# Kernel optimization log

Hardware: AMD Instinct MI355X
Metric: run time of the kernel (lower is better)

## Reference

```python
import jax, jax.numpy as jnp
import numpy as np

B, S, D, E, F = 2, 1024, 1024, 14, 2048

def setup_inputs() -> dict:
    key = jax.random.key(0)
    k0, k1, k2, k3 = jax.random.split(key, 4)
    h = jax.random.normal(k0, (B, S, D), jnp.float32)
    gate_w = jax.random.normal(k1, (E, D), jnp.float32) * 0.02
    # kaiming-uniform-ish scale for expert weights
    w1 = jax.random.normal(k2, (E, D, F), jnp.float32) * (1.0 / np.sqrt(D).astype(np.float32))
    b1 = jnp.zeros((E, F), jnp.float32)
    w2 = jax.random.normal(k3, (E, F, D), jnp.float32) * (1.0 / np.sqrt(F).astype(np.float32))
    b2 = jnp.zeros((E, D), jnp.float32)
    return {"h": h, "gate_w": gate_w, "w1": w1, "b1": b1, "w2": w2, "b2": b2}

def reference(h, gate_w, w1, b1, w2, b2):
    # Eval-mode forward (no expert dropout, router_step=None, return_aux=False path)
    Bb, Ss, Dd = h.shape
    x = h.reshape(Bb * Ss, Dd)                       # (N, D)
    logits = x @ gate_w.T                            # (N, E)
    probs = jax.nn.softmax(logits, axis=-1)
    top2_p, top2_i = jax.lax.top_k(probs, 2)         # (N, 2)
    w = top2_p / jnp.maximum(top2_p.sum(-1, keepdims=True), 1e-10)
    # dense all-experts FFN
    hh = jnp.einsum('nd,edf->nef', x, w1) + b1       # (N, E, F)
    hh = jax.nn.gelu(hh, approximate=False)          # torch F.gelu default = exact erf
    all_out = jnp.einsum('nef,efd->ned', hh, w2) + b2  # (N, E, D)
    n = jnp.arange(x.shape[0])
    out0 = all_out[n, top2_i[:, 0]]                  # (N, D)
    out1 = all_out[n, top2_i[:, 1]]
    moe_out = w[:, 0:1] * out0 + w[:, 1:2] * out1
    result = jnp.clip(x + moe_out, -100.0, 100.0).reshape(Bb, Ss, Dd)
    return result
```

## Files before the change

### kernel.cpp

```cpp
#include <hip/hip_runtime.h>
#include <cstdint>
#include <cstddef>

#define NTOK 2048
#define DDIM 1024
#define FDIM 2048
#define NEXP 14
#define MAXT 2048

typedef __attribute__((ext_vector_type(8))) short short8;
typedef __attribute__((ext_vector_type(4))) float floatx4;

__device__ __forceinline__ unsigned pack2bf(float lo, float hi) {
    unsigned a = __float_as_uint(lo), b = __float_as_uint(hi);
    return ((a + 0x8000u) >> 16) | ((b + 0x8000u) & 0xffff0000u);
}
__device__ __forceinline__ unsigned short f2bf1(float f) {
    return (unsigned short)((__float_as_uint(f) + 0x8000u) >> 16);
}

__device__ __forceinline__ void glds16(const void* g, void* lds) {
    __builtin_amdgcn_global_load_lds((const __attribute__((address_space(1))) unsigned*)g,
                                     (__attribute__((address_space(3))) unsigned*)lds, 16, 0, 0);
}

__device__ __forceinline__ int bswz(int n) { return ((n >> 2) ^ n ^ (n >> 4)) & 7; }

__global__ __launch_bounds__(256) void cvtx_kernel(const float* __restrict__ x,
                                                   unsigned short* __restrict__ xb,
                                                   int* __restrict__ cnt) {
    if (blockIdx.x == 0 && threadIdx.x < NEXP) cnt[threadIdx.x] = 0;
    const size_t i = ((size_t)blockIdx.x * 256 + threadIdx.x) * 8;
    float4 a = *(const float4*)(x + i);
    float4 b = *(const float4*)(x + i + 4);
    uint4 u;
    u.x = pack2bf(a.x, a.y); u.y = pack2bf(a.z, a.w);
    u.z = pack2bf(b.x, b.y); u.w = pack2bf(b.z, b.w);
    *(uint4*)(xb + i) = u;
}

__global__ __launch_bounds__(256) void gate_kernel(
    const float* __restrict__ x, const float* __restrict__ gw,
    int* __restrict__ cnt, int* __restrict__ lists, float* __restrict__ wt)
{
    const int wave = threadIdx.x >> 6, lane = threadIdx.x & 63;
    const int n = blockIdx.x * 4 + wave;
    float part[NEXP];
#pragma unroll
    for (int e = 0; e < NEXP; ++e) part[e] = 0.f;
    const float4* xr = (const float4*)(x + (size_t)n * DDIM);
#pragma unroll
    for (int kk = 0; kk < 4; ++kk) {
        const float4 xv = xr[kk * 64 + lane];
#pragma unroll
        for (int e = 0; e < NEXP; ++e) {
            const float4 g = ((const float4*)(gw + e * DDIM))[kk * 64 + lane];
            part[e] = fmaf(xv.x, g.x, fmaf(xv.y, g.y, fmaf(xv.z, g.z, fmaf(xv.w, g.w, part[e]))));
        }
    }
#pragma unroll
    for (int e = 0; e < NEXP; ++e) {
        float v = part[e];
        for (int off = 32; off; off >>= 1) v += __shfl_xor(v, off);
        part[e] = v;
    }
    int i0 = 0; float l0 = part[0];
#pragma unroll
    for (int e = 1; e < NEXP; ++e) if (part[e] > l0) { l0 = part[e]; i0 = e; }
    int i1 = -1; float l1 = -3.0e38f;
#pragma unroll
    for (int e = 0; e < NEXP; ++e) if (e != i0 && part[e] > l1) { l1 = part[e]; i1 = e; }
    if (lane == 0) {
        const float r  = __expf(l1 - l0);
        wt[2 * n]     = 1.f / (1.f + r);
        wt[2 * n + 1] = r / (1.f + r);
        int p0 = atomicAdd(&cnt[i0], 1); lists[i0 * MAXT + p0] = 2 * n;
        int p1 = atomicAdd(&cnt[i1], 1); lists[i1 * MAXT + p1] = 2 * n + 1;
    }
}

#define MAXJOBS 78
__global__ void jobs_kernel(const int* __restrict__ cnt, int* __restrict__ job_e,
                            int* __restrict__ job_mt, int* __restrict__ njobs) {
    if (threadIdx.x == 0) {
        int J = 0;
        for (int e = 0; e < NEXP; ++e) {
            const int m = (cnt[e] + 63) >> 6;
            for (int i = 0; i < m; ++i) { job_e[J] = e; job_mt[J] = i; ++J; }
        }
        njobs[0] = J;
    }
}

__global__ __launch_bounds__(256) void gemm1_kernel(
    const unsigned short* __restrict__ xb, const float* __restrict__ w1,
    const float* __restrict__ b1, const int* __restrict__ cnt,
    const int* __restrict__ lists, const int* __restrict__ job_e,
    const int* __restrict__ job_mt, const int* __restrict__ njobs,
    unsigned short* __restrict__ hh)
{
    const int j = blockIdx.y;
    if (j >= njobs[0]) return;
    const int e = job_e[j], mt = job_mt[j], nt = blockIdx.x;
    const int count = cnt[e];
    const int* list = lists + e * MAXT + mt * 64;
    const int mloc = min(64, count - mt * 64);

    __shared__ __align__(16) unsigned short As[2][64 * 64];
    __shared__ __align__(16) unsigned short Bs[2][128 * 64];

    const int t = threadIdx.x, lane = t & 63, wave = t >> 6;
    const int lrow = lane & 15, lq = lane >> 4;
    const int wm = (wave & 1) * 32, wn = (wave >> 1) * 64;

    const int achk = (lane & 7) ^ (lane >> 3);
    const int r0 = wave * 16 + (lane >> 3);
    const unsigned short* aG0 = xb + (size_t)(list[min(r0, mloc - 1)] >> 1) * DDIM + achk * 8;
    const unsigned short* aG1 = xb + (size_t)(list[min(r0 + 8, mloc - 1)] >> 1) * DDIM + achk * 8;

    const int n4 = (t & 31) * 4, kg = t >> 5;
    const float* bG = w1 + (size_t)e * DDIM * FDIM + nt * 128 + n4;

    floatx4 acc[2][4];
#pragma unroll
    for (int i = 0; i < 2; ++i)
#pragma unroll
        for (int jn = 0; jn < 4; ++jn) acc[i][jn] = (floatx4)0.f;

    floatx4 brv[8];
    glds16(aG0, &As[0][(wave * 16) * 64]);
    glds16(aG1, &As[0][(wave * 16 + 8) * 64]);
#pragma unroll
    for (int jj = 0; jj < 8; ++jj)
        brv[jj] = *(const floatx4*)(bG + (size_t)(kg * 8 + jj) * FDIM);
#pragma unroll
    for (int nn = 0; nn < 4; ++nn) {
        const int n = n4 + nn, slot = kg ^ bswz(n);
        uint4 u;
        u.x = pack2bf(brv[0][nn], brv[1][nn]); u.y = pack2bf(brv[2][nn], brv[3][nn]);
        u.z = pack2bf(brv[4][nn], brv[5][nn]); u.w = pack2bf(brv[6][nn], brv[7][nn]);
        *(uint4*)&Bs[0][n * 64 + slot * 8] = u;
    }
#pragma unroll
    for (int jj = 0; jj < 8; ++jj)
        brv[jj] = *(const floatx4*)(bG + (size_t)(64 + kg * 8 + jj) * FDIM);

    int p = 0;
    for (int k0 = 0; k0 < DDIM; k0 += 64) {
        __syncthreads();
        if (k0 + 64 < DDIM) {
            glds16(aG0 + k0 + 64, &As[p ^ 1][(wave * 16) * 64]);
            glds16(aG1 + k0 + 64, &As[p ^ 1][(wave * 16 + 8) * 64]);
#pragma unroll
            for (int nn = 0; nn < 4; ++nn) {
                const int n = n4 + nn, slot = kg ^ bswz(n);
                uint4 u;
                u.x = pack2bf(brv[0][nn], brv[1][nn]); u.y = pack2bf(brv[2][nn], brv[3][nn]);
                u.z = pack2bf(brv[4][nn], brv[5][nn]); u.w = pack2bf(brv[6][nn], brv[7][nn]);
                *(uint4*)&Bs[p ^ 1][n * 64 + slot * 8] = u;
            }
        }
        if (k0 + 128 < DDIM) {
#pragma unroll
            for (int jj = 0; jj < 8; ++jj)
                brv[jj] = *(const floatx4*)(bG + (size_t)(k0 + 128 + kg * 8 + jj) * FDIM);
        }
#pragma unroll
        for (int ks = 0; ks < 2; ++ks) {
            const int c = ks * 4 + lq;
            short8 af[2], bf[4];
#pragma unroll
            for (int i = 0; i < 2; ++i) {
                const int r = wm + i * 16 + lrow;
                af[i] = *(const short8*)&As[p][r * 64 + ((c ^ (r & 7)) * 8)];
            }
#pragma unroll
            for (int jn = 0; jn < 4; ++jn) {
                const int n = wn + jn * 16 + lrow;
                bf[jn] = *(const short8*)&Bs[p][n * 64 + ((c ^ bswz(n)) * 8)];
            }
#pragma unroll
            for (int i = 0; i < 2; ++i)
#pragma unroll
                for (int jn = 0; jn < 4; ++jn)
                    acc[i][jn] = __builtin_amdgcn_mfma_f32_16x16x32_bf16(af[i], bf[jn], acc[i][jn], 0, 0, 0);
        }
        p ^= 1;
    }
#pragma unroll
    for (int jn = 0; jn < 4; ++jn) {
        const int n = nt * 128 + wn + jn * 16 + lrow;
        const float bias = b1[e * FDIM + n];
#pragma unroll
        for (int i = 0; i < 2; ++i) {
#pragma unroll
            for (int r = 0; r < 4; ++r) {
                const int m = wm + i * 16 + lq * 4 + r;
                if (m < mloc) {
                    const int pp = list[m];
                    float v = acc[i][jn][r] + bias;
                    v = 0.5f * v * (1.0f + erff(v * 0.70710678118654752f));
                    hh[(size_t)pp * FDIM + n] = f2bf1(v);
                }
            }
        }
    }
}

__global__ __launch_bounds__(256) void gemm2_kernel(
    const unsigned short* __restrict__ hh, const float* __restrict__ w2,
    const float* __restrict__ b2, const int* __restrict__ cnt,
    const int* __restrict__ lists, const int* __restrict__ job_e,
    const int* __restrict__ job_mt, const int* __restrict__ njobs,
    const float* __restrict__ wt, float* __restrict__ out0, float* __restrict__ out1)
{
    const int j = blockIdx.y;
    if (j >= njobs[0]) return;
    const int e = job_e[j], mt = job_mt[j], nt = blockIdx.x;
    const int count = cnt[e];
    const int* list = lists + e * MAXT + mt * 64;
    const int mloc = min(64, count - mt * 64);

    __shared__ __align__(16) unsigned short As[2][64 * 64];
    __shared__ __align__(16) unsigned short Bs[2][128 * 64];

    const int t = threadIdx.x, lane = t & 63, wave = t >> 6;
    const int lrow = lane & 15, lq = lane >> 4;
    const int wm = (wave & 1) * 32, wn = (wave >> 1) * 64;

    const int achk = (lane & 7) ^ (lane >> 3);
    const int r0 = wave * 16 + (lane >> 3);
    const unsigned short* aG0 = hh + (size_t)list[min(r0, mloc - 1)] * FDIM + achk * 8;
    const unsigned short* aG1 = hh + (size_t)list[min(r0 + 8, mloc - 1)] * FDIM + achk * 8;

    const int n4 = (t & 31) * 4, kg = t >> 5;
    const float* bG = w2 + (size_t)e * FDIM * DDIM + nt * 128 + n4;

    floatx4 acc[2][4];
#pragma unroll
    for (int i = 0; i < 2; ++i)
#pragma unroll
        for (int jn = 0; jn < 4; ++jn) acc[i][jn] = (floatx4)0.f;

    floatx4 brv[8];
    glds16(aG0, &As[0][(wave * 16) * 64]);
    glds16(aG1, &As[0][(wave * 16 + 8) * 64]);
#pragma unroll
    for (int jj = 0; jj < 8; ++jj)
        brv[jj] = *(const floatx4*)(bG + (size_t)(kg * 8 + jj) * DDIM);
#pragma unroll
    for (int nn = 0; nn < 4; ++nn) {
        const int n = n4 + nn, slot = kg ^ bswz(n);
        uint4 u;
        u.x = pack2bf(brv[0][nn], brv[1][nn]); u.y = pack2bf(brv[2][nn], brv[3][nn]);
        u.z = pack2bf(brv[4][nn], brv[5][nn]); u.w = pack2bf(brv[6][nn], brv[7][nn]);
        *(uint4*)&Bs[0][n * 64 + slot * 8] = u;
    }
#pragma unroll
    for (int jj = 0; jj < 8; ++jj)
        brv[jj] = *(const floatx4*)(bG + (size_t)(64 + kg * 8 + jj) * DDIM);

    int p = 0;
    for (int k0 = 0; k0 < FDIM; k0 += 64) {
        __syncthreads();
        if (k0 + 64 < FDIM) {
            glds16(aG0 + k0 + 64, &As[p ^ 1][(wave * 16) * 64]);
            glds16(aG1 + k0 + 64, &As[p ^ 1][(wave * 16 + 8) * 64]);
#pragma unroll
            for (int nn = 0; nn < 4; ++nn) {
                const int n = n4 + nn, slot = kg ^ bswz(n);
                uint4 u;
                u.x = pack2bf(brv[0][nn], brv[1][nn]); u.y = pack2bf(brv[2][nn], brv[3][nn]);
                u.z = pack2bf(brv[4][nn], brv[5][nn]); u.w = pack2bf(brv[6][nn], brv[7][nn]);
                *(uint4*)&Bs[p ^ 1][n * 64 + slot * 8] = u;
            }
        }
        if (k0 + 128 < FDIM) {
#pragma unroll
            for (int jj = 0; jj < 8; ++jj)
                brv[jj] = *(const floatx4*)(bG + (size_t)(k0 + 128 + kg * 8 + jj) * DDIM);
        }
#pragma unroll
        for (int ks = 0; ks < 2; ++ks) {
            const int c = ks * 4 + lq;
            short8 af[2], bf[4];
#pragma unroll
            for (int i = 0; i < 2; ++i) {
                const int r = wm + i * 16 + lrow;
                af[i] = *(const short8*)&As[p][r * 64 + ((c ^ (r & 7)) * 8)];
            }
#pragma unroll
            for (int jn = 0; jn < 4; ++jn) {
                const int n = wn + jn * 16 + lrow;
                bf[jn] = *(const short8*)&Bs[p][n * 64 + ((c ^ bswz(n)) * 8)];
            }
#pragma unroll
            for (int i = 0; i < 2; ++i)
#pragma unroll
                for (int jn = 0; jn < 4; ++jn)
                    acc[i][jn] = __builtin_amdgcn_mfma_f32_16x16x32_bf16(af[i], bf[jn], acc[i][jn], 0, 0, 0);
        }
        p ^= 1;
    }
#pragma unroll
    for (int jn = 0; jn < 4; ++jn) {
        const int n = nt * 128 + wn + jn * 16 + lrow;
        const float bias = b2[e * DDIM + n];
#pragma unroll
        for (int i = 0; i < 2; ++i) {
#pragma unroll
            for (int r = 0; r < 4; ++r) {
                const int m = wm + i * 16 + lq * 4 + r;
                if (m < mloc) {
                    const int pp = list[m];
                    const int tok = pp >> 1;
                    const float v = (acc[i][jn][r] + bias) * wt[pp];
                    float* dst = (pp & 1) ? out1 : out0;
                    dst[(size_t)tok * DDIM + n] = v;
                }
            }
        }
    }
}

__global__ __launch_bounds__(256) void finalize_kernel(
    const float* __restrict__ x, const float* __restrict__ o1,
    float* __restrict__ out)
{
    const size_t i = ((size_t)blockIdx.x * 256 + threadIdx.x) * 4;
    float4 xv = *(const float4*)(x + i);
    float4 a  = *(const float4*)(out + i);
    float4 b  = *(const float4*)(o1 + i);
    float4 r;
    r.x = fminf(fmaxf(xv.x + a.x + b.x, -100.f), 100.f);
    r.y = fminf(fmaxf(xv.y + a.y + b.y, -100.f), 100.f);
    r.z = fminf(fmaxf(xv.z + a.z + b.z, -100.f), 100.f);
    r.w = fminf(fmaxf(xv.w + a.w + b.w, -100.f), 100.f);
    *(float4*)(out + i) = r;
}

extern "C" void kernel_launch(void* const* d_in, const int* in_sizes, int n_in,
                              void* d_out, int out_size, void* d_ws, size_t ws_size,
                              hipStream_t stream) {
    const float* h  = (const float*)d_in[0];
    const float* gw = (const float*)d_in[1];
    const float* w1 = (const float*)d_in[2];
    const float* b1 = (const float*)d_in[3];
    const float* w2 = (const float*)d_in[4];
    const float* b2 = (const float*)d_in[5];
    float* out = (float*)d_out;

    char* ws = (char*)d_ws;
    int*   cnt    = (int*)ws;
    int*   lists  = (int*)(ws + 256);
    float* wt     = (float*)(ws + 114944);
    int*   job_e  = (int*)(ws + 131328);
    int*   job_mt = (int*)(ws + 131840);
    int*   njobs  = (int*)(ws + 132352);
    unsigned short* xb = (unsigned short*)(ws + 262144);
    float* o1     = (float*)(ws + 262144 + 4194304);
    unsigned short* hhb = (unsigned short*)(ws + 262144 + 4194304 + 8388608);

    cvtx_kernel<<<NTOK * DDIM / (256 * 8), 256, 0, stream>>>(h, xb, cnt);
    gate_kernel<<<NTOK / 4, 256, 0, stream>>>(h, gw, cnt, lists, wt);
    jobs_kernel<<<1, 64, 0, stream>>>(cnt, job_e, job_mt, njobs);
    gemm1_kernel<<<dim3(FDIM / 128, MAXJOBS), 256, 0, stream>>>(xb, w1, b1, cnt, lists, job_e, job_mt, njobs, hhb);
    gemm2_kernel<<<dim3(DDIM / 128, MAXJOBS), 256, 0, stream>>>(hhb, w2, b2, cnt, lists, job_e, job_mt, njobs, wt, out, o1);
    finalize_kernel<<<NTOK * DDIM / (256 * 4), 256, 0, stream>>>(h, o1, out);
}
```

Before: 414.7 us.

## Software-pipeline expert GEMM main loops with partial waitcnt and MFMA priority

Both expert GEMM K-loops are rewritten as a manually unrolled two-stage pipeline with ping-pong register buffers for the fp32 weight prefetch. Each step waits with `s_waitcnt vmcnt(8)` before a raw `s_barrier`, rather than a full `__syncthreads`. This lets the next tile's weight global loads stay in flight across the barrier, hiding memory latency behind MFMA work. Sched barriers fix the instruction order, `s_setprio` raises wave priority around the MFMA bursts, and launch bounds request 3 blocks per CU. The risks are higher register pressure from the doubled prefetch buffers and correctness relying on hand-counted vmcnt values.

```diff
diff --git a/kernel.cpp b/kernel.cpp
--- a/kernel.cpp
+++ b/kernel.cpp
@@ -25,6 +25,8 @@
 }
 
 __device__ __forceinline__ int bswz(int n) { return ((n >> 2) ^ n ^ (n >> 4)) & 7; }
+
+#define SBAR() __builtin_amdgcn_sched_barrier(0)
 
 __global__ __launch_bounds__(256) void cvtx_kernel(const float* __restrict__ x,
                                                    unsigned short* __restrict__ xb,
@@ -92,7 +94,49 @@
     }
 }
 
-__global__ __launch_bounds__(256) void gemm1_kernel(
+#define LOADB(dst, kbase, STRIDE) {                                           \
+    _Pragma("unroll") for (int jj = 0; jj < 8; ++jj)                          \
+        dst[jj] = *(const floatx4*)(bG + (size_t)((kbase) + kg * 8 + jj) * (STRIDE)); }
+
+#define WRITEB(src, buf) {                                                    \
+    _Pragma("unroll") for (int nn = 0; nn < 4; ++nn) {                        \
+        const int n_ = n4 + nn, slot_ = kg ^ bswz(n_);                        \
+        uint4 u_;                                                             \
+        u_.x = pack2bf(src[0][nn], src[1][nn]); u_.y = pack2bf(src[2][nn], src[3][nn]); \
+        u_.z = pack2bf(src[4][nn], src[5][nn]); u_.w = pack2bf(src[6][nn], src[7][nn]); \
+        *(uint4*)&Bs[buf][n_ * 64 + slot_ * 8] = u_; } }
+
+#define STAGEA(buf, koff) {                                                   \
+    glds16(aG0 + (koff), &As[buf][(wave * 16) * 64]);                         \
+    glds16(aG1 + (koff), &As[buf][(wave * 16 + 8) * 64]); }
+
+#define COMPUTE(buf) {                                                        \
+    _Pragma("unroll") for (int ks = 0; ks < 2; ++ks) {                        \
+        const int c_ = ks * 4 + lq;                                           \
+        short8 af[2], bf[4];                                                  \
+        _Pragma("unroll") for (int ii = 0; ii < 2; ++ii) {                    \
+            const int r_ = wm + ii * 16 + lrow;                               \
+            af[ii] = *(const short8*)&As[buf][r_ * 64 + ((c_ ^ (r_ & 7)) * 8)]; } \
+        _Pragma("unroll") for (int jn = 0; jn < 4; ++jn) {                    \
+            const int n_ = wn + jn * 16 + lrow;                               \
+            bf[jn] = *(const short8*)&Bs[buf][n_ * 64 + ((c_ ^ bswz(n_)) * 8)]; } \
+        __builtin_amdgcn_s_setprio(1);                                        \
+        _Pragma("unroll") for (int ii = 0; ii < 2; ++ii)                      \
+            _Pragma("unroll") for (int jn = 0; jn < 4; ++jn)                  \
+                acc[ii][jn] = __builtin_amdgcn_mfma_f32_16x16x32_bf16(af[ii], bf[jn], acc[ii][jn], 0, 0, 0); \
+        __builtin_amdgcn_s_setprio(0); } }
+
+#define STEADY(i, curbuf, brv_c, brv_n, STRIDE) {                             \
+    STAGEA((curbuf) ^ 1, ((i) + 1) * 64);                                     \
+    WRITEB(brv_c, (curbuf) ^ 1);                                              \
+    SBAR();                                                                   \
+    LOADB(brv_n, ((i) + 2) * 64, STRIDE);                                     \
+    SBAR();                                                                   \
+    COMPUTE(curbuf);                                                          \
+    asm volatile("s_waitcnt vmcnt(8) lgkmcnt(0)" ::: "memory");               \
+    __builtin_amdgcn_s_barrier(); }
+
+__global__ __launch_bounds__(256, 3) void gemm1_kernel(
     const unsigned short* __restrict__ xb, const float* __restrict__ w1,
     const float* __restrict__ b1, const int* __restrict__ cnt,
     const int* __restrict__ lists, const int* __restrict__ job_e,
@@ -123,82 +167,47 @@
 
     floatx4 acc[2][4];
 #pragma unroll
-    for (int i = 0; i < 2; ++i)
-#pragma unroll
-        for (int jn = 0; jn < 4; ++jn) acc[i][jn] = (floatx4)0.f;
-
-    floatx4 brv[8];
-    glds16(aG0, &As[0][(wave * 16) * 64]);
-    glds16(aG1, &As[0][(wave * 16 + 8) * 64]);
-#pragma unroll
-    for (int jj = 0; jj < 8; ++jj)
-        brv[jj] = *(const floatx4*)(bG + (size_t)(kg * 8 + jj) * FDIM);
-#pragma unroll
-    for (int nn = 0; nn < 4; ++nn) {
-        const int n = n4 + nn, slot = kg ^ bswz(n);
-        uint4 u;
-        u.x = pack2bf(brv[0][nn], brv[1][nn]); u.y = pack2bf(brv[2][nn], brv[3][nn]);
-        u.z = pack2bf(brv[4][nn], brv[5][nn]); u.w = pack2bf(brv[6][nn], brv[7][nn]);
-        *(uint4*)&Bs[0][n * 64 + slot * 8] = u;
-    }
-#pragma unroll
-    for (int jj = 0; jj < 8; ++jj)
-        brv[jj] = *(const floatx4*)(bG + (size_t)(64 + kg * 8 + jj) * FDIM);
-
-    int p = 0;
-    for (int k0 = 0; k0 < DDIM; k0 += 64) {
-        __syncthreads();
-        if (k0 + 64 < DDIM) {
-            glds16(aG0 + k0 + 64, &As[p ^ 1][(wave * 16) * 64]);
-            glds16(aG1 + k0 + 64, &As[p ^ 1][(wave * 16 + 8) * 64]);
-#pragma unroll
-            for (int nn = 0; nn < 4; ++nn) {
-                const int n = n4 + nn, slot = kg ^ bswz(n);
-                uint4 u;
-                u.x = pack2bf(brv[0][nn], brv[1][nn]); u.y = pack2bf(brv[2][nn], brv[3][nn]);
-                u.z = pack2bf(brv[4][nn], brv[5][nn]); u.w = pack2bf(brv[6][nn], brv[7][nn]);
-                *(uint4*)&Bs[p ^ 1][n * 64 + slot * 8] = u;
-            }
-        }
-        if (k0 + 128 < DDIM) {
-#pragma unroll
-            for (int jj = 0; jj < 8; ++jj)
-                brv[jj] = *(const floatx4*)(bG + (size_t)(k0 + 128 + kg * 8 + jj) * FDIM);
-        }
-#pragma unroll
-        for (int ks = 0; ks < 2; ++ks) {
-            const int c = ks * 4 + lq;
-            short8 af[2], bf[4];
-#pragma unroll
-            for (int i = 0; i < 2; ++i) {
-                const int r = wm + i * 16 + lrow;
-                af[i] = *(const short8*)&As[p][r * 64 + ((c ^ (r & 7)) * 8)];
-            }
-#pragma unroll
-            for (int jn = 0; jn < 4; ++jn) {
-                const int n = wn + jn * 16 + lrow;
-                bf[jn] = *(const short8*)&Bs[p][n * 64 + ((c ^ bswz(n)) * 8)];
-            }
-#pragma unroll
-            for (int i = 0; i < 2; ++i)
-#pragma unroll
-                for (int jn = 0; jn < 4; ++jn)
-                    acc[i][jn] = __builtin_amdgcn_mfma_f32_16x16x32_bf16(af[i], bf[jn], acc[i][jn], 0, 0, 0);
-        }
-        p ^= 1;
-    }
+    for (int ii = 0; ii < 2; ++ii)
+#pragma unroll
+        for (int jn = 0; jn < 4; ++jn) acc[ii][jn] = (floatx4)0.f;
+
+    floatx4 brvA[8], brvB[8];
+
+    STAGEA(0, 0);
+    SBAR();
+    LOADB(brvB, 0, FDIM);
+    WRITEB(brvB, 0);
+    SBAR();
+    LOADB(brvA, 64, FDIM);
+    asm volatile("s_waitcnt vmcnt(8) lgkmcnt(0)" ::: "memory");
+    __builtin_amdgcn_s_barrier();
+
+#pragma unroll 1
+    for (int it = 0; it < 7; ++it) {
+        const int i = it * 2;
+        STEADY(i, 0, brvA, brvB, FDIM);
+        STEADY(i + 1, 1, brvB, brvA, FDIM);
+    }
+    STAGEA(1, 15 * 64);
+    WRITEB(brvA, 1);
+    SBAR();
+    COMPUTE(0);
+    asm volatile("s_waitcnt vmcnt(0) lgkmcnt(0)" ::: "memory");
+    __builtin_amdgcn_s_barrier();
+    COMPUTE(1);
+
 #pragma unroll
     for (int jn = 0; jn < 4; ++jn) {
         const int n = nt * 128 + wn + jn * 16 + lrow;
         const float bias = b1[e * FDIM + n];
 #pragma unroll
-        for (int i = 0; i < 2; ++i) {
+        for (int ii = 0; ii < 2; ++ii) {
 #pragma unroll
             for (int r = 0; r < 4; ++r) {
-                const int m = wm + i * 16 + lq * 4 + r;
+                const int m = wm + ii * 16 + lq * 4 + r;
                 if (m < mloc) {
                     const int pp = list[m];
-                    float v = acc[i][jn][r] + bias;
+                    float v = acc[ii][jn][r] + bias;
                     v = 0.5f * v * (1.0f + erff(v * 0.70710678118654752f));
                     hh[(size_t)pp * FDIM + n] = f2bf1(v);
                 }
@@ -207,7 +216,7 @@
     }
 }
 
-__global__ __launch_bounds__(256) void gemm2_kernel(
+__global__ __launch_bounds__(256, 3) void gemm2_kernel(
     const unsigned short* __restrict__ hh, const float* __restrict__ w2,
     const float* __restrict__ b2, const int* __restrict__ cnt,
     const int* __restrict__ lists, const int* __restrict__ job_e,
@@ -238,83 +247,48 @@
 
     floatx4 acc[2][4];
 #pragma unroll
-    for (int i = 0; i < 2; ++i)
-#pragma unroll
-        for (int jn = 0; jn < 4; ++jn) acc[i][jn] = (floatx4)0.f;
-
-    floatx4 brv[8];
-    glds16(aG0, &As[0][(wave * 16) * 64]);
-    glds16(aG1, &As[0][(wave * 16 + 8) * 64]);
-#pragma unroll
-    for (int jj = 0; jj < 8; ++jj)
-        brv[jj] = *(const floatx4*)(bG + (size_t)(kg * 8 + jj) * DDIM);
-#pragma unroll
-    for (int nn = 0; nn < 4; ++nn) {
-        const int n = n4 + nn, slot = kg ^ bswz(n);
-        uint4 u;
-        u.x = pack2bf(brv[0][nn], brv[1][nn]); u.y = pack2bf(brv[2][nn], brv[3][nn]);
-        u.z = pack2bf(brv[4][nn], brv[5][nn]); u.w = pack2bf(brv[6][nn], brv[7][nn]);
-        *(uint4*)&Bs[0][n * 64 + slot * 8] = u;
-    }
-#pragma unroll
-    for (int jj = 0; jj < 8; ++jj)
-        brv[jj] = *(const floatx4*)(bG + (size_t)(64 + kg * 8 + jj) * DDIM);
-
-    int p = 0;
-    for (int k0 = 0; k0 < FDIM; k0 += 64) {
-        __syncthreads();
-        if (k0 + 64 < FDIM) {
-            glds16(aG0 + k0 + 64, &As[p ^ 1][(wave * 16) * 64]);
-            glds16(aG1 + k0 + 64, &As[p ^ 1][(wave * 16 + 8) * 64]);
-#pragma unroll
-            for (int nn = 0; nn < 4; ++nn) {
-                const int n = n4 + nn, slot = kg ^ bswz(n);
-                uint4 u;
-                u.x = pack2bf(brv[0][nn], brv[1][nn]); u.y = pack2bf(brv[2][nn], brv[3][nn]);
-                u.z = pack2bf(brv[4][nn], brv[5][nn]); u.w = pack2bf(brv[6][nn], brv[7][nn]);
-                *(uint4*)&Bs[p ^ 1][n * 64 + slot * 8] = u;
-            }
-        }
-        if (k0 + 128 < FDIM) {
-#pragma unroll
-            for (int jj = 0; jj < 8; ++jj)
-                brv[jj] = *(const floatx4*)(bG + (size_t)(k0 + 128 + kg * 8 + jj) * DDIM);
-        }
-#pragma unroll
-        for (int ks = 0; ks < 2; ++ks) {
-            const int c = ks * 4 + lq;
-            short8 af[2], bf[4];
-#pragma unroll
-            for (int i = 0; i < 2; ++i) {
-                const int r = wm + i * 16 + lrow;
-                af[i] = *(const short8*)&As[p][r * 64 + ((c ^ (r & 7)) * 8)];
-            }
-#pragma unroll
-            for (int jn = 0; jn < 4; ++jn) {
-                const int n = wn + jn * 16 + lrow;
-                bf[jn] = *(const short8*)&Bs[p][n * 64 + ((c ^ bswz(n)) * 8)];
-            }
-#pragma unroll
-            for (int i = 0; i < 2; ++i)
-#pragma unroll
-                for (int jn = 0; jn < 4; ++jn)
-                    acc[i][jn] = __builtin_amdgcn_mfma_f32_16x16x32_bf16(af[i], bf[jn], acc[i][jn], 0, 0, 0);
-        }
-        p ^= 1;
-    }
+    for (int ii = 0; ii < 2; ++ii)
+#pragma unroll
+        for (int jn = 0; jn < 4; ++jn) acc[ii][jn] = (floatx4)0.f;
+
+    floatx4 brvA[8], brvB[8];
+
+    STAGEA(0, 0);
+    SBAR();
+    LOADB(brvB, 0, DDIM);
+    WRITEB(brvB, 0);
+    SBAR();
+    LOADB(brvA, 64, DDIM);
+    asm volatile("s_waitcnt vmcnt(8) lgkmcnt(0)" ::: "memory");
+    __builtin_amdgcn_s_barrier();
+
+#pragma unroll 1
+    for (int it = 0; it < 15; ++it) {
+        const int i = it * 2;
+        STEADY(i, 0, brvA, brvB, DDIM);
+        STEADY(i + 1, 1, brvB, brvA, DDIM);
+    }
+    STAGEA(1, 31 * 64);
+    WRITEB(brvA, 1);
+    SBAR();
+    COMPUTE(0);
+    asm volatile("s_waitcnt vmcnt(0) lgkmcnt(0)" ::: "memory");
+    __builtin_amdgcn_s_barrier();
+    COMPUTE(1);
+
 #pragma unroll
     for (int jn = 0; jn < 4; ++jn) {
         const int n = nt * 128 + wn + jn * 16 + lrow;
         const float bias = b2[e * DDIM + n];
 #pragma unroll
-        for (int i = 0; i < 2; ++i) {
+        for (int ii = 0; ii < 2; ++ii) {
 #pragma unroll
             for (int r = 0; r < 4; ++r) {
-                const int m = wm + i * 16 + lq * 4 + r;
+                const int m = wm + ii * 16 + lq * 4 + r;
                 if (m < mloc) {
                     const int pp = list[m];
                     const int tok = pp >> 1;
-                    const float v = (acc[i][jn][r] + bias) * wt[pp];
+                    const float v = (acc[ii][jn][r] + bias) * wt[pp];
                     float* dst = (pp & 1) ? out1 : out0;
                     dst[(size_t)tok * DDIM + n] = v;
                 }
```

Result: no change. 420.2 us (+1.3%).
